# Performance work log

Hardware: AMD Instinct MI355X
Metric: run time of the kernel (lower is better)

## Reference

```python
import jax, jax.numpy as jnp
import numpy as np

N_NODES = 10000
N_EDGES = 640000
D = 128


def setup_inputs() -> dict:
    key = jax.random.key(0)
    ks = jax.random.split(key, 8)
    x = jax.random.normal(ks[0], (N_NODES, D), dtype=jnp.float32)
    edge_weight = jax.random.uniform(ks[1], (N_EDGES,), dtype=jnp.float32)
    W0 = jax.random.normal(ks[2], (D, D), dtype=jnp.float32) * (1.0 / np.sqrt(D))
    b0 = jnp.zeros((D,), dtype=jnp.float32)
    W1 = jax.random.normal(ks[3], (D, D), dtype=jnp.float32) * (1.0 / np.sqrt(D))
    b1 = jnp.zeros((D,), dtype=jnp.float32)
    src = jax.random.randint(ks[4], (N_EDGES,), 0, N_NODES)
    dst = jax.random.randint(ks[5], (N_EDGES,), 0, N_NODES)
    return {"x": x, "edge_weight": edge_weight, "W0": W0, "b0": b0,
            "W1": W1, "b1": b1, "src": src, "dst": dst}


def _graph_conv(h, src, dst, edge_weight, W, b):
    # DGL GraphConv with norm='both', bias, activation=relu.
    n = h.shape[0]
    ones = jnp.ones((src.shape[0],), dtype=h.dtype)
    out_deg = jax.ops.segment_sum(ones, src, num_segments=n)
    in_deg = jax.ops.segment_sum(ones, dst, num_segments=n)
    norm_src = jax.lax.rsqrt(jnp.maximum(out_deg, 1.0))  # [N]
    norm_dst = jax.lax.rsqrt(jnp.maximum(in_deg, 1.0))   # [N]
    h = h * norm_src[:, None]
    # gather -> weight edges -> scatter-add (sparse neighbor aggregation)
    msg = h[src] * edge_weight[:, None]                  # [E, D]
    agg = jax.ops.segment_sum(msg, dst, num_segments=n)  # [N, D]
    rst = agg @ W                                        # in_feats == out_feats: aggregate first
    rst = rst * norm_dst[:, None] + b
    return jax.nn.relu(rst)  # activation inside GraphConv


def reference(x, edge_weight, W0, b0, W1, b1, src, dst):
    # NET.forward (full-graph path): per layer GraphConv -> activation -> dropout.
    # Dropout is identity in eval mode; outer relu after GraphConv's internal relu is idempotent
    # but applied for faithfulness.
    h = jax.nn.relu(_graph_conv(x, src, dst, edge_weight, W0, b0))
    h = jax.nn.relu(_graph_conv(h, src, dst, edge_weight, W1, b1))
    return h  # predict is None (n_classes=None)
```

## Files before the change

### kernel.cpp

```cpp
#include <hip/hip_runtime.h>

#define D 128
#define NB 256
#define Q 8
#define BQ (NB / Q)
#define NBINS_MAX 10016
#define GM 32

__global__ __launch_bounds__(256) void hist_kernel(const int* __restrict__ src, const int* __restrict__ dst,
                                                   int* __restrict__ pd, unsigned short* __restrict__ ps,
                                                   int E, int n) {
    __shared__ int hd[NBINS_MAX];
    __shared__ int hs[NBINS_MAX];
    int b = blockIdx.x, t = threadIdx.x;
    int chunk = (E + NB - 1) / NB;
    int e0 = b * chunk, e1 = min(e0 + chunk, E);
    for (int i = t; i < n; i += 256) { hd[i] = 0; hs[i] = 0; }
    __syncthreads();
    for (int e = e0 + t; e < e1; e += 256) {
        atomicAdd(&hd[dst[e]], 1);
        atomicAdd(&hs[src[e]], 1);
    }
    __syncthreads();
    for (int i = t; i < n; i += 256) {
        pd[(size_t)b * n + i] = hd[i];
        ps[(size_t)b * n + i] = (unsigned short)hs[i];
    }
}

__global__ __launch_bounds__(256) void colscan_kernel(int* __restrict__ pd, const unsigned short* __restrict__ ps,
                                                      int* __restrict__ qtot_d, int* __restrict__ qtot_s, int n) {
    int bin = blockIdx.x * 256 + threadIdx.x;
    int q = blockIdx.y;
    if (bin >= n) return;
    int b0 = q * BQ;
    int run = 0, ssum = 0;
#pragma unroll 8
    for (int j = 0; j < BQ; ++j) {
        size_t idx = (size_t)(b0 + j) * n + bin;
        int v = pd[idx];
        pd[idx] = run;
        run += v;
        ssum += (int)ps[idx];
    }
    qtot_d[(size_t)q * n + bin] = run;
    qtot_s[(size_t)q * n + bin] = ssum;
}

__global__ __launch_bounds__(256) void finalize_kernel(int* __restrict__ qtot_d ,
                                                       const int* __restrict__ qtot_s,
                                                       int* __restrict__ in_deg,
                                                       float* __restrict__ norm_src, float* __restrict__ norm_dst,
                                                       int n) {
    int bin = blockIdx.x * 256 + threadIdx.x;
    if (bin >= n) return;
    int run = 0;
#pragma unroll
    for (int q = 0; q < Q; ++q) {
        size_t i = (size_t)q * n + bin;
        int v = qtot_d[i];
        qtot_d[i] = run;
        run += v;
    }
    in_deg[bin] = run;
    norm_dst[bin] = rsqrtf(fmaxf((float)run, 1.0f));
    int tot = 0;
#pragma unroll
    for (int q = 0; q < Q; ++q) tot += qtot_s[(size_t)q * n + bin];
    norm_src[bin] = rsqrtf(fmaxf((float)tot, 1.0f));
}

__global__ __launch_bounds__(1024) void scan_kernel(const int* __restrict__ in_deg, int* __restrict__ row_start, int n) {
    __shared__ int buf[NBINS_MAX];
    __shared__ int part[1024];
    int t = threadIdx.x;
    for (int i = t; i < n; i += 1024) buf[i] = in_deg[i];
    __syncthreads();
    int ipt = (n + 1023) / 1024;
    int lo = min(t * ipt, n), hi = min(lo + ipt, n);
    int s = 0;
    for (int i = lo; i < hi; ++i) s += buf[i];
    part[t] = s;
    __syncthreads();
    for (int off = 1; off < 1024; off <<= 1) {
        int v = 0;
        if (t >= off) v = part[t - off];
        __syncthreads();
        if (t >= off) part[t] += v;
        __syncthreads();
    }
    int run = part[t] - s;
    for (int i = lo; i < hi; ++i) {
        int v = buf[i];
        buf[i] = run;
        run += v;
    }
    __syncthreads();
    for (int i = t; i < n; i += 1024) row_start[i] = buf[i];
    if (t == 0) row_start[n] = part[1023];
}

__global__ __launch_bounds__(256) void fill_kernel(const int* __restrict__ src, const int* __restrict__ dst,
                                                   const float* __restrict__ ew, const float* __restrict__ ns,
                                                   const int* __restrict__ row_start, const int* __restrict__ qbase,
                                                   const int* __restrict__ pd,
                                                   int2* __restrict__ sorted, int E, int n) {
    __shared__ int cursor[NBINS_MAX];
    int b = blockIdx.x, t = threadIdx.x;
    int q = b / BQ;
    int chunk = (E + NB - 1) / NB;
    int e0 = b * chunk, e1 = min(e0 + chunk, E);
    for (int i = t; i < n; i += 256)
        cursor[i] = row_start[i] + qbase[(size_t)q * n + i] + pd[(size_t)b * n + i];
    __syncthreads();
    for (int e = e0 + t; e < e1; e += 256) {
        int d = dst[e];
        int slot = atomicAdd(&cursor[d], 1);
        int s = src[e];
        int2 rec;
        rec.x = s;
        rec.y = __float_as_int(ew[e] * ns[s]);
        sorted[slot] = rec;
    }
}

__global__ __launch_bounds__(256) void agg_kernel(const float* __restrict__ h, const int* __restrict__ row_start,
                                                  const int2* __restrict__ sorted, float* __restrict__ out,
                                                  int n, int qn) {
    int slot  = blockIdx.x & 7;
    int g     = blockIdx.x >> 3;
    int chunk = slot >> 2;
    int quad  = slot & 3;
    int wave  = threadIdx.x >> 6;
    int lane  = threadIdx.x & 63;
    int node  = quad * qn + g * 4 + wave;
    int hiN   = min((quad + 1) * qn, n);
    if (node >= hiN) return;
    const float* hc = h + chunk * 64 + lane;
    int beg = __builtin_amdgcn_readfirstlane(row_start[node]);
    int end = __builtin_amdgcn_readfirstlane(row_start[node + 1]);
    float acc = 0.f;
    int s = beg;
    if (s < end && (s & 1)) {
        int2 rr = sorted[s];
        acc = fmaf(__int_as_float(rr.y), hc[rr.x << 7], acc);
        ++s;
    }
    int4 p0, p1, p2, p3;
    if (s + 8 <= end) {
        p0 = *(const int4*)(sorted + s);
        p1 = *(const int4*)(sorted + s + 2);
        p2 = *(const int4*)(sorted + s + 4);
        p3 = *(const int4*)(sorted + s + 6);
    }
    for (; s + 16 <= end; s += 8) {
        int4 q0 = *(const int4*)(sorted + s + 8);
        int4 q1 = *(const int4*)(sorted + s + 10);
        int4 q2 = *(const int4*)(sorted + s + 12);
        int4 q3 = *(const int4*)(sorted + s + 14);
        float x0 = hc[p0.x << 7];
        float x1 = hc[p0.z << 7];
        float x2 = hc[p1.x << 7];
        float x3 = hc[p1.z << 7];
        float x4 = hc[p2.x << 7];
        float x5 = hc[p2.z << 7];
        float x6 = hc[p3.x << 7];
        float x7 = hc[p3.z << 7];
        acc = fmaf(__int_as_float(p0.y), x0, acc);
        acc = fmaf(__int_as_float(p0.w), x1, acc);
        acc = fmaf(__int_as_float(p1.y), x2, acc);
        acc = fmaf(__int_as_float(p1.w), x3, acc);
        acc = fmaf(__int_as_float(p2.y), x4, acc);
        acc = fmaf(__int_as_float(p2.w), x5, acc);
        acc = fmaf(__int_as_float(p3.y), x6, acc);
        acc = fmaf(__int_as_float(p3.w), x7, acc);
        p0 = q0; p1 = q1; p2 = q2; p3 = q3;
    }
    if (s + 8 <= end) {
        float x0 = hc[p0.x << 7];
        float x1 = hc[p0.z << 7];
        float x2 = hc[p1.x << 7];
        float x3 = hc[p1.z << 7];
        float x4 = hc[p2.x << 7];
        float x5 = hc[p2.z << 7];
        float x6 = hc[p3.x << 7];
        float x7 = hc[p3.z << 7];
        acc = fmaf(__int_as_float(p0.y), x0, acc);
        acc = fmaf(__int_as_float(p0.w), x1, acc);
        acc = fmaf(__int_as_float(p1.y), x2, acc);
        acc = fmaf(__int_as_float(p1.w), x3, acc);
        acc = fmaf(__int_as_float(p2.y), x4, acc);
        acc = fmaf(__int_as_float(p2.w), x5, acc);
        acc = fmaf(__int_as_float(p3.y), x6, acc);
        acc = fmaf(__int_as_float(p3.w), x7, acc);
        s += 8;
    }
    for (; s + 2 <= end; s += 2) {
        int4 p = *(const int4*)(sorted + s);
        acc = fmaf(__int_as_float(p.y), hc[p.x << 7], acc);
        acc = fmaf(__int_as_float(p.w), hc[p.z << 7], acc);
    }
    if (s < end) {
        int2 rr = sorted[s];
        acc = fmaf(__int_as_float(rr.y), hc[rr.x << 7], acc);
    }
    out[((size_t)node << 7) + chunk * 64 + lane] = acc;
}

__global__ __launch_bounds__(256) void gemm_kernel(const float* __restrict__ A, const float* __restrict__ W,
                                                   const float* __restrict__ bias, const float* __restrict__ norm_dst,
                                                   float* __restrict__ out, int n) {
    __shared__ __align__(16) float sAT[D][GM + 2];
    int tid = threadIdx.x;
    int row0 = blockIdx.x * GM;
    for (int i = tid; i < GM * 32; i += 256) {
        int r = i >> 5;
        int kq = i & 31;
        int rr = row0 + r;
        float4 v = make_float4(0.f, 0.f, 0.f, 0.f);
        if (rr < n) v = *(const float4*)(A + (size_t)rr * D + kq * 4);
        sAT[kq * 4 + 0][r] = v.x;
        sAT[kq * 4 + 1][r] = v.y;
        sAT[kq * 4 + 2][r] = v.z;
        sAT[kq * 4 + 3][r] = v.w;
    }
    __syncthreads();
    int tx = tid & 15;
    int ty = tid >> 4;
    int c0 = tx * 8;
    int r0 = ty * 2;
    float acc0[8], acc1[8];
#pragma unroll
    for (int j = 0; j < 8; ++j) { acc0[j] = 0.f; acc1[j] = 0.f; }
    const float* Wk = W + c0;
#pragma unroll 4
    for (int k = 0; k < D; ++k) {
        float2 a = *(const float2*)&sAT[k][r0];
        float4 w0 = *(const float4*)(Wk);
        float4 w1 = *(const float4*)(Wk + 4);
        Wk += D;
        acc0[0] = fmaf(a.x, w0.x, acc0[0]);
        acc0[1] = fmaf(a.x, w0.y, acc0[1]);
        acc0[2] = fmaf(a.x, w0.z, acc0[2]);
        acc0[3] = fmaf(a.x, w0.w, acc0[3]);
        acc0[4] = fmaf(a.x, w1.x, acc0[4]);
        acc0[5] = fmaf(a.x, w1.y, acc0[5]);
        acc0[6] = fmaf(a.x, w1.z, acc0[6]);
        acc0[7] = fmaf(a.x, w1.w, acc0[7]);
        acc1[0] = fmaf(a.y, w0.x, acc1[0]);
        acc1[1] = fmaf(a.y, w0.y, acc1[1]);
        acc1[2] = fmaf(a.y, w0.z, acc1[2]);
        acc1[3] = fmaf(a.y, w0.w, acc1[3]);
        acc1[4] = fmaf(a.y, w1.x, acc1[4]);
        acc1[5] = fmaf(a.y, w1.y, acc1[5]);
        acc1[6] = fmaf(a.y, w1.z, acc1[6]);
        acc1[7] = fmaf(a.y, w1.w, acc1[7]);
    }
    int r = row0 + r0;
    if (r < n) {
        float nd = norm_dst[r];
        float4 o0, o1;
        o0.x = fmaxf(fmaf(acc0[0], nd, bias[c0 + 0]), 0.f);
        o0.y = fmaxf(fmaf(acc0[1], nd, bias[c0 + 1]), 0.f);
        o0.z = fmaxf(fmaf(acc0[2], nd, bias[c0 + 2]), 0.f);
        o0.w = fmaxf(fmaf(acc0[3], nd, bias[c0 + 3]), 0.f);
        o1.x = fmaxf(fmaf(acc0[4], nd, bias[c0 + 4]), 0.f);
        o1.y = fmaxf(fmaf(acc0[5], nd, bias[c0 + 5]), 0.f);
        o1.z = fmaxf(fmaf(acc0[6], nd, bias[c0 + 6]), 0.f);
        o1.w = fmaxf(fmaf(acc0[7], nd, bias[c0 + 7]), 0.f);
        *(float4*)(out + (size_t)r * D + c0) = o0;
        *(float4*)(out + (size_t)r * D + c0 + 4) = o1;
    }
    r = row0 + r0 + 1;
    if (r < n) {
        float nd = norm_dst[r];
        float4 o0, o1;
        o0.x = fmaxf(fmaf(acc1[0], nd, bias[c0 + 0]), 0.f);
        o0.y = fmaxf(fmaf(acc1[1], nd, bias[c0 + 1]), 0.f);
        o0.z = fmaxf(fmaf(acc1[2], nd, bias[c0 + 2]), 0.f);
        o0.w = fmaxf(fmaf(acc1[3], nd, bias[c0 + 3]), 0.f);
        o1.x = fmaxf(fmaf(acc1[4], nd, bias[c0 + 4]), 0.f);
        o1.y = fmaxf(fmaf(acc1[5], nd, bias[c0 + 5]), 0.f);
        o1.z = fmaxf(fmaf(acc1[6], nd, bias[c0 + 6]), 0.f);
        o1.w = fmaxf(fmaf(acc1[7], nd, bias[c0 + 7]), 0.f);
        *(float4*)(out + (size_t)r * D + c0) = o0;
        *(float4*)(out + (size_t)r * D + c0 + 4) = o1;
    }
}

extern "C" void kernel_launch(void* const* d_in, const int* in_sizes, int n_in,
                              void* d_out, int out_size, void* d_ws, size_t ws_size,
                              hipStream_t stream) {
    const float* x  = (const float*)d_in[0];
    const float* ew = (const float*)d_in[1];
    const float* W0 = (const float*)d_in[2];
    const float* b0 = (const float*)d_in[3];
    const float* W1 = (const float*)d_in[4];
    const float* b1 = (const float*)d_in[5];
    const int* src  = (const int*)d_in[6];
    const int* dst  = (const int*)d_in[7];
    float* out = (float*)d_out;

    int n = in_sizes[0] / D;
    int E = in_sizes[6];
    if (n <= 0 || E <= 0) return;

    char* ws = (char*)d_ws;
    size_t off = 0;
    auto alloc = [&](size_t bytes) -> void* {
        void* p = ws + off;
        off = (off + bytes + 255) & ~(size_t)255;
        return p;
    };
    int* row_start  = (int*)alloc(((size_t)n + 1) * 4);
    int* in_deg     = (int*)alloc((size_t)n * 4);
    float* norm_src = (float*)alloc((size_t)n * 4);
    float* norm_dst = (float*)alloc((size_t)n * 4);
    int* qtot_d     = (int*)alloc((size_t)Q * n * 4);
    int* qtot_s     = (int*)alloc((size_t)Q * n * 4);
    size_t sorted_bytes = (size_t)E * 8;
    size_t ps_bytes = (size_t)NB * n * 2;
    int2* sorted    = (int2*)alloc(sorted_bytes > ps_bytes ? sorted_bytes : ps_bytes);
    float* B1       = (float*)alloc((size_t)n * D * 4);
    float* B2       = (float*)alloc((size_t)n * D * 4);
    int* pd = (int*)B1;
    unsigned short* ps = (unsigned short*)sorted;

    int nb = (n + 255) / 256;
    int qn = (n + 3) / 4;
    int ab = 8 * ((qn + 3) / 4);
    int gb = (n + GM - 1) / GM;

    hist_kernel<<<NB, 256, 0, stream>>>(src, dst, pd, ps, E, n);
    colscan_kernel<<<dim3(nb, Q), 256, 0, stream>>>(pd, ps, qtot_d, qtot_s, n);
    finalize_kernel<<<nb, 256, 0, stream>>>(qtot_d, qtot_s, in_deg, norm_src, norm_dst, n);
    scan_kernel<<<1, 1024, 0, stream>>>(in_deg, row_start, n);
    fill_kernel<<<NB, 256, 0, stream>>>(src, dst, ew, norm_src, row_start, qtot_d, pd, sorted, E, n);

    agg_kernel<<<ab, 256, 0, stream>>>(x, row_start, sorted, B1, n, qn);
    gemm_kernel<<<gb, 256, 0, stream>>>(B1, W0, b0, norm_dst, B2, n);
    agg_kernel<<<ab, 256, 0, stream>>>(B2, row_start, sorted, B1, n, qn);
    gemm_kernel<<<gb, 256, 0, stream>>>(B1, W1, b1, norm_dst, out, n);
}
```

Baseline: 190.7 us.

## Split each wave into four edge groups with float4 gathers in aggregation

The aggregation kernel now splits each 64-lane wave into four quarter-waves. Each quarter-wave handles a different edge and each lane loads a float4 of the 64-feature chunk, where before every lane loaded one float per edge. Partial sums are combined at the end with cross-lane shuffles, and only 16 lanes write the result. The aim is to raise memory-level parallelism and issue fewer, wider gather instructions per edge, at the cost of shuffle reductions and a masked tail loop that reads a clamped index.

After: 202.8 us. 1.06x slower.

```diff
diff --git a/kernel.cpp b/kernel.cpp
--- a/kernel.cpp
+++ b/kernel.cpp
@@ -136,75 +136,73 @@
     int node  = quad * qn + g * 4 + wave;
     int hiN   = min((quad + 1) * qn, n);
     if (node >= hiN) return;
-    const float* hc = h + chunk * 64 + lane;
+    int qtr = lane >> 4;
+    int f4  = lane & 15;
+    const float* hc = h + chunk * 64 + f4 * 4;
     int beg = __builtin_amdgcn_readfirstlane(row_start[node]);
     int end = __builtin_amdgcn_readfirstlane(row_start[node + 1]);
-    float acc = 0.f;
+    float4 acc = make_float4(0.f, 0.f, 0.f, 0.f);
     int s = beg;
-    if (s < end && (s & 1)) {
-        int2 rr = sorted[s];
-        acc = fmaf(__int_as_float(rr.y), hc[rr.x << 7], acc);
-        ++s;
-    }
-    int4 p0, p1, p2, p3;
-    if (s + 8 <= end) {
-        p0 = *(const int4*)(sorted + s);
-        p1 = *(const int4*)(sorted + s + 2);
-        p2 = *(const int4*)(sorted + s + 4);
-        p3 = *(const int4*)(sorted + s + 6);
-    }
-    for (; s + 16 <= end; s += 8) {
-        int4 q0 = *(const int4*)(sorted + s + 8);
-        int4 q1 = *(const int4*)(sorted + s + 10);
-        int4 q2 = *(const int4*)(sorted + s + 12);
-        int4 q3 = *(const int4*)(sorted + s + 14);
-        float x0 = hc[p0.x << 7];
-        float x1 = hc[p0.z << 7];
-        float x2 = hc[p1.x << 7];
-        float x3 = hc[p1.z << 7];
-        float x4 = hc[p2.x << 7];
-        float x5 = hc[p2.z << 7];
-        float x6 = hc[p3.x << 7];
-        float x7 = hc[p3.z << 7];
-        acc = fmaf(__int_as_float(p0.y), x0, acc);
-        acc = fmaf(__int_as_float(p0.w), x1, acc);
-        acc = fmaf(__int_as_float(p1.y), x2, acc);
-        acc = fmaf(__int_as_float(p1.w), x3, acc);
-        acc = fmaf(__int_as_float(p2.y), x4, acc);
-        acc = fmaf(__int_as_float(p2.w), x5, acc);
-        acc = fmaf(__int_as_float(p3.y), x6, acc);
-        acc = fmaf(__int_as_float(p3.w), x7, acc);
-        p0 = q0; p1 = q1; p2 = q2; p3 = q3;
-    }
-    if (s + 8 <= end) {
-        float x0 = hc[p0.x << 7];
-        float x1 = hc[p0.z << 7];
-        float x2 = hc[p1.x << 7];
-        float x3 = hc[p1.z << 7];
-        float x4 = hc[p2.x << 7];
-        float x5 = hc[p2.z << 7];
-        float x6 = hc[p3.x << 7];
-        float x7 = hc[p3.z << 7];
-        acc = fmaf(__int_as_float(p0.y), x0, acc);
-        acc = fmaf(__int_as_float(p0.w), x1, acc);
-        acc = fmaf(__int_as_float(p1.y), x2, acc);
-        acc = fmaf(__int_as_float(p1.w), x3, acc);
-        acc = fmaf(__int_as_float(p2.y), x4, acc);
-        acc = fmaf(__int_as_float(p2.w), x5, acc);
-        acc = fmaf(__int_as_float(p3.y), x6, acc);
-        acc = fmaf(__int_as_float(p3.w), x7, acc);
-        s += 8;
-    }
-    for (; s + 2 <= end; s += 2) {
-        int4 p = *(const int4*)(sorted + s);
-        acc = fmaf(__int_as_float(p.y), hc[p.x << 7], acc);
-        acc = fmaf(__int_as_float(p.w), hc[p.z << 7], acc);
-    }
-    if (s < end) {
-        int2 rr = sorted[s];
-        acc = fmaf(__int_as_float(rr.y), hc[rr.x << 7], acc);
-    }
-    out[((size_t)node << 7) + chunk * 64 + lane] = acc;
+    int2 r0, r1, r2, r3;
+    if (s + 16 <= end) {
+        r0 = sorted[s + qtr];
+        r1 = sorted[s + 4 + qtr];
+        r2 = sorted[s + 8 + qtr];
+        r3 = sorted[s + 12 + qtr];
+    }
+    for (; s + 32 <= end; s += 16) {
+        int2 q0 = sorted[s + 16 + qtr];
+        int2 q1 = sorted[s + 20 + qtr];
+        int2 q2 = sorted[s + 24 + qtr];
+        int2 q3 = sorted[s + 28 + qtr];
+        float4 v0 = *(const float4*)(hc + ((size_t)r0.x << 7));
+        float4 v1 = *(const float4*)(hc + ((size_t)r1.x << 7));
+        float4 v2 = *(const float4*)(hc + ((size_t)r2.x << 7));
+        float4 v3 = *(const float4*)(hc + ((size_t)r3.x << 7));
+        float w0 = __int_as_float(r0.y), w1 = __int_as_float(r1.y);
+        float w2 = __int_as_float(r2.y), w3 = __int_as_float(r3.y);
+        acc.x = fmaf(w0, v0.x, acc.x); acc.y = fmaf(w0, v0.y, acc.y);
+        acc.z = fmaf(w0, v0.z, acc.z); acc.w = fmaf(w0, v0.w, acc.w);
+        acc.x = fmaf(w1, v1.x, acc.x); acc.y = fmaf(w1, v1.y, acc.y);
+        acc.z = fmaf(w1, v1.z, acc.z); acc.w = fmaf(w1, v1.w, acc.w);
+        acc.x = fmaf(w2, v2.x, acc.x); acc.y = fmaf(w2, v2.y, acc.y);
+        acc.z = fmaf(w2, v2.z, acc.z); acc.w = fmaf(w2, v2.w, acc.w);
+        acc.x = fmaf(w3, v3.x, acc.x); acc.y = fmaf(w3, v3.y, acc.y);
+        acc.z = fmaf(w3, v3.z, acc.z); acc.w = fmaf(w3, v3.w, acc.w);
+        r0 = q0; r1 = q1; r2 = q2; r3 = q3;
+    }
+    if (s + 16 <= end) {
+        float4 v0 = *(const float4*)(hc + ((size_t)r0.x << 7));
+        float4 v1 = *(const float4*)(hc + ((size_t)r1.x << 7));
+        float4 v2 = *(const float4*)(hc + ((size_t)r2.x << 7));
+        float4 v3 = *(const float4*)(hc + ((size_t)r3.x << 7));
+        float w0 = __int_as_float(r0.y), w1 = __int_as_float(r1.y);
+        float w2 = __int_as_float(r2.y), w3 = __int_as_float(r3.y);
+        acc.x = fmaf(w0, v0.x, acc.x); acc.y = fmaf(w0, v0.y, acc.y);
+        acc.z = fmaf(w0, v0.z, acc.z); acc.w = fmaf(w0, v0.w, acc.w);
+        acc.x = fmaf(w1, v1.x, acc.x); acc.y = fmaf(w1, v1.y, acc.y);
+        acc.z = fmaf(w1, v1.z, acc.z); acc.w = fmaf(w1, v1.w, acc.w);
+        acc.x = fmaf(w2, v2.x, acc.x); acc.y = fmaf(w2, v2.y, acc.y);
+        acc.z = fmaf(w2, v2.z, acc.z); acc.w = fmaf(w2, v2.w, acc.w);
+        acc.x = fmaf(w3, v3.x, acc.x); acc.y = fmaf(w3, v3.y, acc.y);
+        acc.z = fmaf(w3, v3.z, acc.z); acc.w = fmaf(w3, v3.w, acc.w);
+        s += 16;
+    }
+    for (; s < end; s += 4) {
+        int e = s + qtr;
+        int idx = min(e, end - 1);
+        int2 rr = sorted[idx];
+        float w = (e < end) ? __int_as_float(rr.y) : 0.f;
+        float4 v = *(const float4*)(hc + ((size_t)rr.x << 7));
+        acc.x = fmaf(w, v.x, acc.x); acc.y = fmaf(w, v.y, acc.y);
+        acc.z = fmaf(w, v.z, acc.z); acc.w = fmaf(w, v.w, acc.w);
+    }
+    acc.x += __shfl_xor(acc.x, 16); acc.y += __shfl_xor(acc.y, 16);
+    acc.z += __shfl_xor(acc.z, 16); acc.w += __shfl_xor(acc.w, 16);
+    acc.x += __shfl_xor(acc.x, 32); acc.y += __shfl_xor(acc.y, 32);
+    acc.z += __shfl_xor(acc.z, 32); acc.w += __shfl_xor(acc.w, 32);
+    if (lane < 16)
+        *(float4*)(out + ((size_t)node << 7) + chunk * 64 + f4 * 4) = acc;
 }
 
 __global__ __launch_bounds__(256) void gemm_kernel(const float* __restrict__ A, const float* __restrict__ W,
```

## Replace blocked histogram CSR build with global-atomic degree count and fill

Applied to the files above, without the earlier changes.

Drops the per-block shared-memory histogram, column scan and finalize kernels. Degrees are now counted with global atomics after a memset, one scan produces row_start, a cursor copy and both norms, and the fill kernel uses global atomic cursors. This removes several kernel launches and large partial-histogram traffic, at the cost of contended global atomics and a nondeterministic edge order within each row, which can change floating-point summation order.

Measured after the change: 261.1 us. 1.37x slower.

```diff
diff --git a/kernel.cpp b/kernel.cpp
--- a/kernel.cpp
+++ b/kernel.cpp
@@ -1,76 +1,23 @@
 #include <hip/hip_runtime.h>
 
 #define D 128
-#define NB 256
-#define Q 8
-#define BQ (NB / Q)
 #define NBINS_MAX 10016
 #define GM 32
 
-__global__ __launch_bounds__(256) void hist_kernel(const int* __restrict__ src, const int* __restrict__ dst,
-                                                   int* __restrict__ pd, unsigned short* __restrict__ ps,
-                                                   int E, int n) {
-    __shared__ int hd[NBINS_MAX];
-    __shared__ int hs[NBINS_MAX];
-    int b = blockIdx.x, t = threadIdx.x;
-    int chunk = (E + NB - 1) / NB;
-    int e0 = b * chunk, e1 = min(e0 + chunk, E);
-    for (int i = t; i < n; i += 256) { hd[i] = 0; hs[i] = 0; }
-    __syncthreads();
-    for (int e = e0 + t; e < e1; e += 256) {
-        atomicAdd(&hd[dst[e]], 1);
-        atomicAdd(&hs[src[e]], 1);
-    }
-    __syncthreads();
-    for (int i = t; i < n; i += 256) {
-        pd[(size_t)b * n + i] = hd[i];
-        ps[(size_t)b * n + i] = (unsigned short)hs[i];
-    }
-}
-
-__global__ __launch_bounds__(256) void colscan_kernel(int* __restrict__ pd, const unsigned short* __restrict__ ps,
-                                                      int* __restrict__ qtot_d, int* __restrict__ qtot_s, int n) {
-    int bin = blockIdx.x * 256 + threadIdx.x;
-    int q = blockIdx.y;
-    if (bin >= n) return;
-    int b0 = q * BQ;
-    int run = 0, ssum = 0;
-#pragma unroll 8
-    for (int j = 0; j < BQ; ++j) {
-        size_t idx = (size_t)(b0 + j) * n + bin;
-        int v = pd[idx];
-        pd[idx] = run;
-        run += v;
-        ssum += (int)ps[idx];
-    }
-    qtot_d[(size_t)q * n + bin] = run;
-    qtot_s[(size_t)q * n + bin] = ssum;
-}
-
-__global__ __launch_bounds__(256) void finalize_kernel(int* __restrict__ qtot_d ,
-                                                       const int* __restrict__ qtot_s,
-                                                       int* __restrict__ in_deg,
-                                                       float* __restrict__ norm_src, float* __restrict__ norm_dst,
-                                                       int n) {
-    int bin = blockIdx.x * 256 + threadIdx.x;
-    if (bin >= n) return;
-    int run = 0;
-#pragma unroll
-    for (int q = 0; q < Q; ++q) {
-        size_t i = (size_t)q * n + bin;
-        int v = qtot_d[i];
-        qtot_d[i] = run;
-        run += v;
-    }
-    in_deg[bin] = run;
-    norm_dst[bin] = rsqrtf(fmaxf((float)run, 1.0f));
-    int tot = 0;
-#pragma unroll
-    for (int q = 0; q < Q; ++q) tot += qtot_s[(size_t)q * n + bin];
-    norm_src[bin] = rsqrtf(fmaxf((float)tot, 1.0f));
-}
-
-__global__ __launch_bounds__(1024) void scan_kernel(const int* __restrict__ in_deg, int* __restrict__ row_start, int n) {
+__global__ __launch_bounds__(256) void deg_kernel(const int* __restrict__ src, const int* __restrict__ dst,
+                                                  int* __restrict__ in_deg, int* __restrict__ out_deg, int E) {
+    int i = blockIdx.x * 256 + threadIdx.x;
+    int stride = gridDim.x * 256;
+    for (int e = i; e < E; e += stride) {
+        atomicAdd(&in_deg[dst[e]], 1);
+        atomicAdd(&out_deg[src[e]], 1);
+    }
+}
+
+__global__ __launch_bounds__(1024) void scan_kernel(const int* __restrict__ in_deg, const int* __restrict__ out_deg,
+                                                    int* __restrict__ row_start, int* __restrict__ cursor,
+                                                    float* __restrict__ norm_src, float* __restrict__ norm_dst,
+                                                    int n) {
     __shared__ int buf[NBINS_MAX];
     __shared__ int part[1024];
     int t = threadIdx.x;
@@ -96,24 +43,22 @@
         run += v;
     }
     __syncthreads();
-    for (int i = t; i < n; i += 1024) row_start[i] = buf[i];
+    for (int i = t; i < n; i += 1024) {
+        int rs = buf[i];
+        row_start[i] = rs;
+        cursor[i] = rs;
+        norm_dst[i] = rsqrtf(fmaxf((float)in_deg[i], 1.0f));
+        norm_src[i] = rsqrtf(fmaxf((float)out_deg[i], 1.0f));
+    }
     if (t == 0) row_start[n] = part[1023];
 }
 
 __global__ __launch_bounds__(256) void fill_kernel(const int* __restrict__ src, const int* __restrict__ dst,
                                                    const float* __restrict__ ew, const float* __restrict__ ns,
-                                                   const int* __restrict__ row_start, const int* __restrict__ qbase,
-                                                   const int* __restrict__ pd,
-                                                   int2* __restrict__ sorted, int E, int n) {
-    __shared__ int cursor[NBINS_MAX];
-    int b = blockIdx.x, t = threadIdx.x;
-    int q = b / BQ;
-    int chunk = (E + NB - 1) / NB;
-    int e0 = b * chunk, e1 = min(e0 + chunk, E);
-    for (int i = t; i < n; i += 256)
-        cursor[i] = row_start[i] + qbase[(size_t)q * n + i] + pd[(size_t)b * n + i];
-    __syncthreads();
-    for (int e = e0 + t; e < e1; e += 256) {
+                                                   int* __restrict__ cursor, int2* __restrict__ sorted, int E) {
+    int i = blockIdx.x * 256 + threadIdx.x;
+    int stride = gridDim.x * 256;
+    for (int e = i; e < E; e += stride) {
         int d = dst[e];
         int slot = atomicAdd(&cursor[d], 1);
         int s = src[e];
@@ -313,29 +258,25 @@
         return p;
     };
     int* row_start  = (int*)alloc(((size_t)n + 1) * 4);
-    int* in_deg     = (int*)alloc((size_t)n * 4);
+    int* cursor     = (int*)alloc((size_t)n * 4);
+    int* deg_buf    = (int*)alloc((size_t)2 * n * 4);
     float* norm_src = (float*)alloc((size_t)n * 4);
     float* norm_dst = (float*)alloc((size_t)n * 4);
-    int* qtot_d     = (int*)alloc((size_t)Q * n * 4);
-    int* qtot_s     = (int*)alloc((size_t)Q * n * 4);
-    size_t sorted_bytes = (size_t)E * 8;
-    size_t ps_bytes = (size_t)NB * n * 2;
-    int2* sorted    = (int2*)alloc(sorted_bytes > ps_bytes ? sorted_bytes : ps_bytes);
+    int2* sorted    = (int2*)alloc((size_t)E * 8);
     float* B1       = (float*)alloc((size_t)n * D * 4);
     float* B2       = (float*)alloc((size_t)n * D * 4);
-    int* pd = (int*)B1;
-    unsigned short* ps = (unsigned short*)sorted;
-
-    int nb = (n + 255) / 256;
+    int* in_deg  = deg_buf;
+    int* out_deg = deg_buf + n;
+
+    int eb = (E + 255) / 256;
     int qn = (n + 3) / 4;
     int ab = 8 * ((qn + 3) / 4);
     int gb = (n + GM - 1) / GM;
 
-    hist_kernel<<<NB, 256, 0, stream>>>(src, dst, pd, ps, E, n);
-    colscan_kernel<<<dim3(nb, Q), 256, 0, stream>>>(pd, ps, qtot_d, qtot_s, n);
-    finalize_kernel<<<nb, 256, 0, stream>>>(qtot_d, qtot_s, in_deg, norm_src, norm_dst, n);
-    scan_kernel<<<1, 1024, 0, stream>>>(in_deg, row_start, n);
-    fill_kernel<<<NB, 256, 0, stream>>>(src, dst, ew, norm_src, row_start, qtot_d, pd, sorted, E, n);
+    hipMemsetAsync(deg_buf, 0, (size_t)2 * n * 4, stream);
+    deg_kernel<<<eb, 256, 0, stream>>>(src, dst, in_deg, out_deg, E);
+    scan_kernel<<<1, 1024, 0, stream>>>(in_deg, out_deg, row_start, cursor, norm_src, norm_dst, n);
+    fill_kernel<<<eb, 256, 0, stream>>>(src, dst, ew, norm_src, cursor, sorted, E);
 
     agg_kernel<<<ab, 256, 0, stream>>>(x, row_start, sorted, B1, n, qn);
     gemm_kernel<<<gb, 256, 0, stream>>>(B1, W0, b0, norm_dst, B2, n);
```

## Store gathered node features in fp16 and deepen gather unroll to 16

Applied to the files above, without the earlier changes.

Adds a cast kernel that converts input features to half precision, and makes the first GEMM write its output in fp16, so both aggregation passes gather 2-byte values instead of 4-byte ones. The goal is to halve gather bandwidth and cache footprint in the memory-bound edge aggregation. The agg loop is also unrolled from 8 to 16 edges per iteration for more loads in flight. Workspace buffers that used to alias are given separate allocations. In exchange it adds an extra kernel launch, loses precision in the features, and uses more registers.

New measurement: 188.5 us. Within noise of the previous version (-1.2%).

```diff
diff --git a/kernel.cpp b/kernel.cpp
--- a/kernel.cpp
+++ b/kernel.cpp
@@ -1,4 +1,5 @@
 #include <hip/hip_runtime.h>
+#include <hip/hip_fp16.h>
 
 #define D 128
 #define NB 256
@@ -6,6 +7,16 @@
 #define BQ (NB / Q)
 #define NBINS_MAX 10016
 #define GM 32
+
+__global__ __launch_bounds__(256) void cast_kernel(const float* __restrict__ x, __half* __restrict__ xh, int total4) {
+    int i = blockIdx.x * 256 + threadIdx.x;
+    if (i >= total4) return;
+    float4 v = *(const float4*)(x + (size_t)i * 4);
+    __half2 a = __floats2half2_rn(v.x, v.y);
+    __half2 b = __floats2half2_rn(v.z, v.w);
+    *(__half2*)(xh + (size_t)i * 4) = a;
+    *(__half2*)(xh + (size_t)i * 4 + 2) = b;
+}
 
 __global__ __launch_bounds__(256) void hist_kernel(const int* __restrict__ src, const int* __restrict__ dst,
                                                    int* __restrict__ pd, unsigned short* __restrict__ ps,
@@ -124,7 +135,7 @@
     }
 }
 
-__global__ __launch_bounds__(256) void agg_kernel(const float* __restrict__ h, const int* __restrict__ row_start,
+__global__ __launch_bounds__(256) void agg_kernel(const __half* __restrict__ h, const int* __restrict__ row_start,
                                                   const int2* __restrict__ sorted, float* __restrict__ out,
                                                   int n, int qn) {
     int slot  = blockIdx.x & 7;
@@ -136,80 +147,121 @@
     int node  = quad * qn + g * 4 + wave;
     int hiN   = min((quad + 1) * qn, n);
     if (node >= hiN) return;
-    const float* hc = h + chunk * 64 + lane;
+    const __half* hc = h + chunk * 64 + lane;
     int beg = __builtin_amdgcn_readfirstlane(row_start[node]);
     int end = __builtin_amdgcn_readfirstlane(row_start[node + 1]);
     float acc = 0.f;
     int s = beg;
     if (s < end && (s & 1)) {
         int2 rr = sorted[s];
-        acc = fmaf(__int_as_float(rr.y), hc[rr.x << 7], acc);
+        acc = fmaf(__int_as_float(rr.y), __half2float(hc[(size_t)rr.x << 7]), acc);
         ++s;
     }
-    int4 p0, p1, p2, p3;
-    if (s + 8 <= end) {
+    int4 p0, p1, p2, p3, p4, p5, p6, p7;
+    if (s + 16 <= end) {
         p0 = *(const int4*)(sorted + s);
         p1 = *(const int4*)(sorted + s + 2);
         p2 = *(const int4*)(sorted + s + 4);
         p3 = *(const int4*)(sorted + s + 6);
-    }
-    for (; s + 16 <= end; s += 8) {
-        int4 q0 = *(const int4*)(sorted + s + 8);
-        int4 q1 = *(const int4*)(sorted + s + 10);
-        int4 q2 = *(const int4*)(sorted + s + 12);
-        int4 q3 = *(const int4*)(sorted + s + 14);
-        float x0 = hc[p0.x << 7];
-        float x1 = hc[p0.z << 7];
-        float x2 = hc[p1.x << 7];
-        float x3 = hc[p1.z << 7];
-        float x4 = hc[p2.x << 7];
-        float x5 = hc[p2.z << 7];
-        float x6 = hc[p3.x << 7];
-        float x7 = hc[p3.z << 7];
-        acc = fmaf(__int_as_float(p0.y), x0, acc);
-        acc = fmaf(__int_as_float(p0.w), x1, acc);
-        acc = fmaf(__int_as_float(p1.y), x2, acc);
-        acc = fmaf(__int_as_float(p1.w), x3, acc);
-        acc = fmaf(__int_as_float(p2.y), x4, acc);
-        acc = fmaf(__int_as_float(p2.w), x5, acc);
-        acc = fmaf(__int_as_float(p3.y), x6, acc);
-        acc = fmaf(__int_as_float(p3.w), x7, acc);
+        p4 = *(const int4*)(sorted + s + 8);
+        p5 = *(const int4*)(sorted + s + 10);
+        p6 = *(const int4*)(sorted + s + 12);
+        p7 = *(const int4*)(sorted + s + 14);
+    }
+    for (; s + 32 <= end; s += 16) {
+        int4 q0 = *(const int4*)(sorted + s + 16);
+        int4 q1 = *(const int4*)(sorted + s + 18);
+        int4 q2 = *(const int4*)(sorted + s + 20);
+        int4 q3 = *(const int4*)(sorted + s + 22);
+        int4 q4 = *(const int4*)(sorted + s + 24);
+        int4 q5 = *(const int4*)(sorted + s + 26);
+        int4 q6 = *(const int4*)(sorted + s + 28);
+        int4 q7 = *(const int4*)(sorted + s + 30);
+        __half x0  = hc[(size_t)p0.x << 7];
+        __half x1  = hc[(size_t)p0.z << 7];
+        __half x2  = hc[(size_t)p1.x << 7];
+        __half x3  = hc[(size_t)p1.z << 7];
+        __half x4  = hc[(size_t)p2.x << 7];
+        __half x5  = hc[(size_t)p2.z << 7];
+        __half x6  = hc[(size_t)p3.x << 7];
+        __half x7  = hc[(size_t)p3.z << 7];
+        __half x8  = hc[(size_t)p4.x << 7];
+        __half x9  = hc[(size_t)p4.z << 7];
+        __half x10 = hc[(size_t)p5.x << 7];
+        __half x11 = hc[(size_t)p5.z << 7];
+        __half x12 = hc[(size_t)p6.x << 7];
+        __half x13 = hc[(size_t)p6.z << 7];
+        __half x14 = hc[(size_t)p7.x << 7];
+        __half x15 = hc[(size_t)p7.z << 7];
+        acc = fmaf(__int_as_float(p0.y), __half2float(x0),  acc);
+        acc = fmaf(__int_as_float(p0.w), __half2float(x1),  acc);
+        acc = fmaf(__int_as_float(p1.y), __half2float(x2),  acc);
+        acc = fmaf(__int_as_float(p1.w), __half2float(x3),  acc);
+        acc = fmaf(__int_as_float(p2.y), __half2float(x4),  acc);
+        acc = fmaf(__int_as_float(p2.w), __half2float(x5),  acc);
+        acc = fmaf(__int_as_float(p3.y), __half2float(x6),  acc);
+        acc = fmaf(__int_as_float(p3.w), __half2float(x7),  acc);
+        acc = fmaf(__int_as_float(p4.y), __half2float(x8),  acc);
+        acc = fmaf(__int_as_float(p4.w), __half2float(x9),  acc);
+        acc = fmaf(__int_as_float(p5.y), __half2float(x10), acc);
+        acc = fmaf(__int_as_float(p5.w), __half2float(x11), acc);
+        acc = fmaf(__int_as_float(p6.y), __half2float(x12), acc);
+        acc = fmaf(__int_as_float(p6.w), __half2float(x13), acc);
+        acc = fmaf(__int_as_float(p7.y), __half2float(x14), acc);
+        acc = fmaf(__int_as_float(p7.w), __half2float(x15), acc);
         p0 = q0; p1 = q1; p2 = q2; p3 = q3;
+        p4 = q4; p5 = q5; p6 = q6; p7 = q7;
+    }
+    if (s + 16 <= end) {
+        acc = fmaf(__int_as_float(p0.y), __half2float(hc[(size_t)p0.x << 7]), acc);
+        acc = fmaf(__int_as_float(p0.w), __half2float(hc[(size_t)p0.z << 7]), acc);
+        acc = fmaf(__int_as_float(p1.y), __half2float(hc[(size_t)p1.x << 7]), acc);
+        acc = fmaf(__int_as_float(p1.w), __half2float(hc[(size_t)p1.z << 7]), acc);
+        acc = fmaf(__int_as_float(p2.y), __half2float(hc[(size_t)p2.x << 7]), acc);
+        acc = fmaf(__int_as_float(p2.w), __half2float(hc[(size_t)p2.z << 7]), acc);
+        acc = fmaf(__int_as_float(p3.y), __half2float(hc[(size_t)p3.x << 7]), acc);
+        acc = fmaf(__int_as_float(p3.w), __half2float(hc[(size_t)p3.z << 7]), acc);
+        acc = fmaf(__int_as_float(p4.y), __half2float(hc[(size_t)p4.x << 7]), acc);
+        acc = fmaf(__int_as_float(p4.w), __half2float(hc[(size_t)p4.z << 7]), acc);
+        acc = fmaf(__int_as_float(p5.y), __half2float(hc[(size_t)p5.x << 7]), acc);
+        acc = fmaf(__int_as_float(p5.w), __half2float(hc[(size_t)p5.z << 7]), acc);
+        acc = fmaf(__int_as_float(p6.y), __half2float(hc[(size_t)p6.x << 7]), acc);
+        acc = fmaf(__int_as_float(p6.w), __half2float(hc[(size_t)p6.z << 7]), acc);
+        acc = fmaf(__int_as_float(p7.y), __half2float(hc[(size_t)p7.x << 7]), acc);
+        acc = fmaf(__int_as_float(p7.w), __half2float(hc[(size_t)p7.z << 7]), acc);
+        s += 16;
     }
     if (s + 8 <= end) {
-        float x0 = hc[p0.x << 7];
-        float x1 = hc[p0.z << 7];
-        float x2 = hc[p1.x << 7];
-        float x3 = hc[p1.z << 7];
-        float x4 = hc[p2.x << 7];
-        float x5 = hc[p2.z << 7];
-        float x6 = hc[p3.x << 7];
-        float x7 = hc[p3.z << 7];
-        acc = fmaf(__int_as_float(p0.y), x0, acc);
-        acc = fmaf(__int_as_float(p0.w), x1, acc);
-        acc = fmaf(__int_as_float(p1.y), x2, acc);
-        acc = fmaf(__int_as_float(p1.w), x3, acc);
-        acc = fmaf(__int_as_float(p2.y), x4, acc);
-        acc = fmaf(__int_as_float(p2.w), x5, acc);
-        acc = fmaf(__int_as_float(p3.y), x6, acc);
-        acc = fmaf(__int_as_float(p3.w), x7, acc);
+        int4 a0 = *(const int4*)(sorted + s);
+        int4 a1 = *(const int4*)(sorted + s + 2);
+        int4 a2 = *(const int4*)(sorted + s + 4);
+        int4 a3 = *(const int4*)(sorted + s + 6);
+        acc = fmaf(__int_as_float(a0.y), __half2float(hc[(size_t)a0.x << 7]), acc);
+        acc = fmaf(__int_as_float(a0.w), __half2float(hc[(size_t)a0.z << 7]), acc);
+        acc = fmaf(__int_as_float(a1.y), __half2float(hc[(size_t)a1.x << 7]), acc);
+        acc = fmaf(__int_as_float(a1.w), __half2float(hc[(size_t)a1.z << 7]), acc);
+        acc = fmaf(__int_as_float(a2.y), __half2float(hc[(size_t)a2.x << 7]), acc);
+        acc = fmaf(__int_as_float(a2.w), __half2float(hc[(size_t)a2.z << 7]), acc);
+        acc = fmaf(__int_as_float(a3.y), __half2float(hc[(size_t)a3.x << 7]), acc);
+        acc = fmaf(__int_as_float(a3.w), __half2float(hc[(size_t)a3.z << 7]), acc);
         s += 8;
     }
     for (; s + 2 <= end; s += 2) {
         int4 p = *(const int4*)(sorted + s);
-        acc = fmaf(__int_as_float(p.y), hc[p.x << 7], acc);
-        acc = fmaf(__int_as_float(p.w), hc[p.z << 7], acc);
+        acc = fmaf(__int_as_float(p.y), __half2float(hc[(size_t)p.x << 7]), acc);
+        acc = fmaf(__int_as_float(p.w), __half2float(hc[(size_t)p.z << 7]), acc);
     }
     if (s < end) {
         int2 rr = sorted[s];
-        acc = fmaf(__int_as_float(rr.y), hc[rr.x << 7], acc);
+        acc = fmaf(__int_as_float(rr.y), __half2float(hc[(size_t)rr.x << 7]), acc);
     }
     out[((size_t)node << 7) + chunk * 64 + lane] = acc;
 }
 
+template <int HALF_OUT>
 __global__ __launch_bounds__(256) void gemm_kernel(const float* __restrict__ A, const float* __restrict__ W,
                                                    const float* __restrict__ bias, const float* __restrict__ norm_dst,
-                                                   float* __restrict__ out, int n) {
+                                                   float* __restrict__ out, __half* __restrict__ out_h, int n) {
     __shared__ __align__(16) float sAT[D][GM + 2];
     int tid = threadIdx.x;
     int row0 = blockIdx.x * GM;
@@ -256,35 +308,31 @@
         acc1[6] = fmaf(a.y, w1.z, acc1[6]);
         acc1[7] = fmaf(a.y, w1.w, acc1[7]);
     }
-    int r = row0 + r0;
-    if (r < n) {
+#pragma unroll 2
+    for (int rr = 0; rr < 2; ++rr) {
+        int r = row0 + r0 + rr;
+        if (r >= n) continue;
+        float* acc = rr ? acc1 : acc0;
         float nd = norm_dst[r];
-        float4 o0, o1;
-        o0.x = fmaxf(fmaf(acc0[0], nd, bias[c0 + 0]), 0.f);
-        o0.y = fmaxf(fmaf(acc0[1], nd, bias[c0 + 1]), 0.f);
-        o0.z = fmaxf(fmaf(acc0[2], nd, bias[c0 + 2]), 0.f);
-        o0.w = fmaxf(fmaf(acc0[3], nd, bias[c0 + 3]), 0.f);
-        o1.x = fmaxf(fmaf(acc0[4], nd, bias[c0 + 4]), 0.f);
-        o1.y = fmaxf(fmaf(acc0[5], nd, bias[c0 + 5]), 0.f);
-        o1.z = fmaxf(fmaf(acc0[6], nd, bias[c0 + 6]), 0.f);
-        o1.w = fmaxf(fmaf(acc0[7], nd, bias[c0 + 7]), 0.f);
-        *(float4*)(out + (size_t)r * D + c0) = o0;
-        *(float4*)(out + (size_t)r * D + c0 + 4) = o1;
-    }
-    r = row0 + r0 + 1;
-    if (r < n) {
-        float nd = norm_dst[r];
-        float4 o0, o1;
-        o0.x = fmaxf(fmaf(acc1[0], nd, bias[c0 + 0]), 0.f);
-        o0.y = fmaxf(fmaf(acc1[1], nd, bias[c0 + 1]), 0.f);
-        o0.z = fmaxf(fmaf(acc1[2], nd, bias[c0 + 2]), 0.f);
-        o0.w = fmaxf(fmaf(acc1[3], nd, bias[c0 + 3]), 0.f);
-        o1.x = fmaxf(fmaf(acc1[4], nd, bias[c0 + 4]), 0.f);
-        o1.y = fmaxf(fmaf(acc1[5], nd, bias[c0 + 5]), 0.f);
-        o1.z = fmaxf(fmaf(acc1[6], nd, bias[c0 + 6]), 0.f);
-        o1.w = fmaxf(fmaf(acc1[7], nd, bias[c0 + 7]), 0.f);
-        *(float4*)(out + (size_t)r * D + c0) = o0;
-        *(float4*)(out + (size_t)r * D + c0 + 4) = o1;
+        float o[8];
+#pragma unroll
+        for (int j = 0; j < 8; ++j) o[j] = fmaxf(fmaf(acc[j], nd, bias[c0 + j]), 0.f);
+        if (HALF_OUT) {
+            __half2 h0 = __floats2half2_rn(o[0], o[1]);
+            __half2 h1 = __floats2half2_rn(o[2], o[3]);
+            __half2 h2 = __floats2half2_rn(o[4], o[5]);
+            __half2 h3 = __floats2half2_rn(o[6], o[7]);
+            __half* p = out_h + (size_t)r * D + c0;
+            *(__half2*)(p + 0) = h0;
+            *(__half2*)(p + 2) = h1;
+            *(__half2*)(p + 4) = h2;
+            *(__half2*)(p + 6) = h3;
+        } else {
+            float4 o0 = make_float4(o[0], o[1], o[2], o[3]);
+            float4 o1 = make_float4(o[4], o[5], o[6], o[7]);
+            *(float4*)(out + (size_t)r * D + c0) = o0;
+            *(float4*)(out + (size_t)r * D + c0 + 4) = o1;
+        }
     }
 }
 
@@ -318,27 +366,28 @@
     float* norm_dst = (float*)alloc((size_t)n * 4);
     int* qtot_d     = (int*)alloc((size_t)Q * n * 4);
     int* qtot_s     = (int*)alloc((size_t)Q * n * 4);
-    size_t sorted_bytes = (size_t)E * 8;
-    size_t ps_bytes = (size_t)NB * n * 2;
-    int2* sorted    = (int2*)alloc(sorted_bytes > ps_bytes ? sorted_bytes : ps_bytes);
+    int2* sorted    = (int2*)alloc((size_t)E * 8);
+    int* pd         = (int*)alloc((size_t)NB * n * 4);
+    unsigned short* ps = (unsigned short*)alloc((size_t)NB * n * 2);
     float* B1       = (float*)alloc((size_t)n * D * 4);
-    float* B2       = (float*)alloc((size_t)n * D * 4);
-    int* pd = (int*)B1;
-    unsigned short* ps = (unsigned short*)sorted;
+    __half* xh      = (__half*)alloc((size_t)n * D * 2);
+    __half* B2h     = (__half*)alloc((size_t)n * D * 2);
 
     int nb = (n + 255) / 256;
     int qn = (n + 3) / 4;
     int ab = 8 * ((qn + 3) / 4);
     int gb = (n + GM - 1) / GM;
-
+    int cb = ((n * D / 4) + 255) / 256;
+
+    cast_kernel<<<cb, 256, 0, stream>>>(x, xh, n * D / 4);
     hist_kernel<<<NB, 256, 0, stream>>>(src, dst, pd, ps, E, n);
     colscan_kernel<<<dim3(nb, Q), 256, 0, stream>>>(pd, ps, qtot_d, qtot_s, n);
     finalize_kernel<<<nb, 256, 0, stream>>>(qtot_d, qtot_s, in_deg, norm_src, norm_dst, n);
     scan_kernel<<<1, 1024, 0, stream>>>(in_deg, row_start, n);
     fill_kernel<<<NB, 256, 0, stream>>>(src, dst, ew, norm_src, row_start, qtot_d, pd, sorted, E, n);
 
-    agg_kernel<<<ab, 256, 0, stream>>>(x, row_start, sorted, B1, n, qn);
-    gemm_kernel<<<gb, 256, 0, stream>>>(B1, W0, b0, norm_dst, B2, n);
-    agg_kernel<<<ab, 256, 0, stream>>>(B2, row_start, sorted, B1, n, qn);
-    gemm_kernel<<<gb, 256, 0, stream>>>(B1, W1, b1, norm_dst, out, n);
-}
+    agg_kernel<<<ab, 256, 0, stream>>>(xh, row_start, sorted, B1, n, qn);
+    gemm_kernel<1><<<gb, 256, 0, stream>>>(B1, W0, b0, norm_dst, nullptr, B2h, n);
+    agg_kernel<<<ab, 256, 0, stream>>>(B2h, row_start, sorted, B1, n, qn);
+    gemm_kernel<0><<<gb, 256, 0, stream>>>(B1, W1, b1, norm_dst, out, nullptr, n);
+}
```
